# Optimization experiments

Measured on AMD Instinct MI355X. Metric: run time of the kernel, lower is better.

The kernel has to match this reference:

```python
import jax, jax.numpy as jnp
import numpy as np

FILTERS = 64
NBITS = 4
NUE = 4
NSPU = 2
NST = NUE * NSPU           # 8 streams total
OUT_CH = NST * NBITS       # 32 output channels
NBS, NANT = 1, 16
CIN = NBS * NANT * 2 + NBS * NANT * NUE * NSPU * 2 + NUE * NSPU + 1  # 297


def hard_sigmoid(x):
    # Keras ConvLSTM2D default recurrent_activation
    return jnp.clip(0.2 * x + 0.5, 0.0, 1.0)


def conv2d(x, w):
    # x: [N,H,W,C], w: [kh,kw,Cin,Cout], SAME padding
    return jax.lax.conv_general_dilated(x, w, (1, 1), 'SAME',
                                        dimension_numbers=('NHWC', 'HWIO', 'NHWC'))


def convlstm2d(x, Wx, Wh, b):
    """Keras ConvLSTM2D (return_sequences=True), gate order i,f,c,o.
    x: [B,T,H,W,Cin] -> [B,T,H,W,F].
    Input-to-hidden convs are precomputed for all timesteps at once;
    only the cheap hidden-to-hidden conv is inside the scan."""
    B, T, H, W, Cin = x.shape
    F = Wh.shape[2]
    xz = conv2d(x.reshape(B * T, H, W, Cin), Wx).reshape(B, T, H, W, 4 * F) + b
    xz = jnp.moveaxis(xz, 1, 0)  # [T,B,H,W,4F]
    h0 = jnp.zeros((B, H, W, F), x.dtype)

    def step(carry, z_in):
        h, c = carry
        z = z_in + conv2d(h, Wh)
        zi, zf, zg, zo = jnp.split(z, 4, axis=-1)
        i = hard_sigmoid(zi)
        f = hard_sigmoid(zf)
        g = jnp.tanh(zg)
        o = hard_sigmoid(zo)
        c = f * c + i * g
        h = o * jnp.tanh(c)
        return (h, c), h

    _, hs = jax.lax.scan(step, (h0, h0), xz)
    return jnp.moveaxis(hs, 0, 1)  # [B,T,H,W,F]


def _lstm_params(key, cin, f, scale=0.05):
    k1, k2, k3 = jax.random.split(key, 3)
    Wx = jax.random.normal(k1, (3, 3, cin, 4 * f), jnp.float32) * scale
    Wh = jax.random.normal(k2, (3, 3, f, 4 * f), jnp.float32) * scale
    b = jax.random.normal(k3, (4 * f,), jnp.float32) * scale
    return Wx, Wh, b


def setup_inputs() -> dict:
    key = jax.random.key(0)
    ks = jax.random.split(key, 10)
    B, T, W = 2, 14, 1536
    inp = {
        'y_ri': jax.random.normal(ks[0], (B, NBS, NANT, T, W, 2), jnp.float32),
        'h_ri': jax.random.normal(ks[1], (B, NBS, NANT, NUE, NSPU, T, W, 2), jnp.float32),
        'err_var': jax.random.uniform(ks[2], (1, 1, 1, NUE, NSPU, T, W), jnp.float32),
        'no': jax.random.uniform(ks[3], (1,), jnp.float32),
    }
    inp['Wx_in'], inp['Wh_in'], inp['b_in'] = _lstm_params(ks[4], CIN, FILTERS)
    inp['Wx_r0'], inp['Wh_r0'], inp['b_r0'] = _lstm_params(ks[5], FILTERS, FILTERS)
    inp['Wx_r1'], inp['Wh_r1'], inp['b_r1'] = _lstm_params(ks[6], FILTERS, FILTERS)
    inp['Wx_out'], inp['Wh_out'], inp['b_out'] = _lstm_params(ks[7], FILTERS, OUT_CH)
    return inp


def _forward(y_ri, h_ri, err_var, no,
             Wx_in, Wh_in, b_in,
             Wx_r0, Wh_r0, b_r0,
             Wx_r1, Wh_r1, b_r1,
             Wx_out, Wh_out, b_out):
    B, nbs, nant, T, W, _ = y_ri.shape
    # y: [B,nbs,nant,T,W,2] -> [B,T,W,nbs*nant*2]
    y_feats = jnp.transpose(y_ri, (0, 3, 4, 1, 2, 5)).reshape(B, T, W, -1)
    # h: [B,nbs,nant,ue,spu,T,W,2] -> [B,T,W,nbs*nant*ue*spu*2]
    h_feats = jnp.transpose(h_ri, (0, 5, 6, 1, 2, 3, 4, 7)).reshape(B, T, W, -1)
    # err_var: [1,1,1,ue,spu,T,W] -> [B,T,W,ue*spu]
    ev = jnp.transpose(err_var[0, 0, 0], (2, 3, 0, 1)).reshape(1, T, W, NUE * NSPU)
    err_feats = jnp.broadcast_to(ev, (B, T, W, NUE * NSPU))
    no_feat = jnp.broadcast_to(no.reshape(1, 1, 1, 1), (B, T, W, 1))
    z = jnp.concatenate([y_feats, h_feats, err_feats, no_feat], axis=-1)
    z = z[:, :, :, None, :]  # [B,T,W,1,C]

    z = convlstm2d(z, Wx_in, Wh_in, b_in)
    # residual blocks (in_ch == filters, so identity skip)
    z = convlstm2d(z, Wx_r0, Wh_r0, b_r0) + z
    z = convlstm2d(z, Wx_r1, Wh_r1, b_r1) + z
    z = convlstm2d(z, Wx_out, Wh_out, b_out)

    z = z[:, :, :, 0, :]  # [B,T,W,OUT_CH]
    N = T * W
    z = z.reshape(B, N, NUE, NSPU, NBITS)
    z = jnp.transpose(z, (0, 2, 3, 1, 4))
    return z.reshape(B, NUE, NSPU, N * NBITS)


def reference(y_ri, h_ri, err_var, no,
              Wx_in, Wh_in, b_in,
              Wx_r0, Wh_r0, b_r0,
              Wx_r1, Wh_r1, b_r1,
              Wx_out, Wh_out, b_out):
    return _forward(y_ri, h_ri, err_var, no,
                    Wx_in, Wh_in, b_in,
                    Wx_r0, Wh_r0, b_r0,
                    Wx_r1, Wh_r1, b_r1,
                    Wx_out, Wh_out, b_out)
```

## Files before the change

### kernel.cpp

```cpp
#include <hip/hip_runtime.h>
#include <hip/hip_bf16.h>


#define BB   2
#define TT   14
#define LL   1536
#define CINR 297
#define CP_IN 320
#define NSTRIP 96
#define NBLK  (BB * NSTRIP)
#define WIN  48

typedef __attribute__((ext_vector_type(8))) short short8;
typedef __attribute__((ext_vector_type(4))) float floatx4;

static constexpr size_t U_WBIN_HI  = 0;
static constexpr size_t U_WBIN_LO  = 245760;
static constexpr size_t U_WBR0_HI  = 491520;
static constexpr size_t U_WBR0_LO  = 540672;
static constexpr size_t U_WBR1_HI  = 589824;
static constexpr size_t U_WBR1_LO  = 638976;
static constexpr size_t U_WBOUT_HI = 688128;
static constexpr size_t U_WBOUT_LO = 712704;
static constexpr size_t U_WHTIN    = 737280;
static constexpr size_t U_WHTR0    = 786432;
static constexpr size_t U_WHTR1    = 835584;
static constexpr size_t U_WHTOUT   = 884736;
static constexpr size_t OFF_BIN   = 448512;
static constexpr size_t OFF_BR0   = 448768;
static constexpr size_t OFF_BR1   = 449024;
static constexpr size_t OFF_BOUT  = 449280;
static constexpr size_t OFF_Z0HI  = 458752;
static constexpr size_t SZ_Z0PL   = 6881280;
static constexpr size_t OFF_Z0LO  = OFF_Z0HI + SZ_Z0PL;
static constexpr size_t OFF_XZ    = OFF_Z0LO + SZ_Z0PL;
static constexpr size_t SZ_XZ     = (size_t)BB*TT*LL*256;
static constexpr size_t OFF_SEQ   = OFF_Z0HI;
static constexpr size_t OFF_SEQHI = OFF_SEQ + (size_t)BB*TT*LL*64;
static constexpr size_t OFF_SEQLO = OFF_SEQHI + (size_t)BB*TT*LL*32;

__device__ __forceinline__ float hsig(float x) {
    return fminf(fmaxf(0.2f * x + 0.5f, 0.0f), 1.0f);
}
__device__ __forceinline__ float ftanh(float x) {
    float e = __expf(2.0f * x);
    return 1.0f - 2.0f / (e + 1.0f);
}
__device__ __forceinline__ unsigned short f2bf(float x) {
    unsigned int u = __builtin_bit_cast(unsigned int, x);
    u += 0x7fffu + ((u >> 16) & 1u);
    return (unsigned short)(u >> 16);
}
__device__ __forceinline__ float bf2f(unsigned short h) {
    unsigned int u = ((unsigned int)h) << 16;
    return __builtin_bit_cast(float, u);
}

__global__ __launch_bounds__(256)
void prep_weights_kernel(const float* wx_in, const float* wh_in, const float* b_in,
                         const float* wx_r0, const float* wh_r0, const float* b_r0,
                         const float* wx_r1, const float* wh_r1, const float* b_r1,
                         const float* wx_out, const float* wh_out, const float* b_out,
                         float* __restrict__ ws)
{
    int idx = blockIdx.x * 256 + threadIdx.x;
    unsigned short* u = (unsigned short*)ws;
    if (idx < 245760) {
        int n = idx / 960, k = idx % 960;
        int kh = k / CP_IN, ci = k % CP_IN;
        float v = 0.0f;
        if (ci < CINR) {
            int f = n >> 2, g = n & 3;
            v = wx_in[((size_t)(kh * 3 + 1) * CINR + ci) * 256 + g * 64 + f];
        }
        unsigned short hi = f2bf(v);
        u[U_WBIN_HI + idx] = hi;
        u[U_WBIN_LO + idx] = f2bf(v - bf2f(hi));
        return;
    }
    idx -= 245760;
    if (idx < 49152) {
        int n = idx / 192, k = idx % 192;
        int kh = k >> 6, ci = k & 63;
        int f = n >> 2, g = n & 3;
        float v = wx_r0[((size_t)(kh * 3 + 1) * 64 + ci) * 256 + g * 64 + f];
        unsigned short hi = f2bf(v);
        u[U_WBR0_HI + idx] = hi;
        u[U_WBR0_LO + idx] = f2bf(v - bf2f(hi));
        return;
    }
    idx -= 49152;
    if (idx < 49152) {
        int n = idx / 192, k = idx % 192;
        int kh = k >> 6, ci = k & 63;
        int f = n >> 2, g = n & 3;
        float v = wx_r1[((size_t)(kh * 3 + 1) * 64 + ci) * 256 + g * 64 + f];
        unsigned short hi = f2bf(v);
        u[U_WBR1_HI + idx] = hi;
        u[U_WBR1_LO + idx] = f2bf(v - bf2f(hi));
        return;
    }
    idx -= 49152;
    if (idx < 24576) {
        int n = idx / 192, k = idx % 192;
        int kh = k >> 6, ci = k & 63;
        int f = n >> 2, g = n & 3;
        float v = wx_out[((size_t)(kh * 3 + 1) * 64 + ci) * 128 + g * 32 + f];
        unsigned short hi = f2bf(v);
        u[U_WBOUT_HI + idx] = hi;
        u[U_WBOUT_LO + idx] = f2bf(v - bf2f(hi));
        return;
    }
    idx -= 24576;
    if (idx < 49152) {
        int n = idx / 192, k = idx % 192, kh = k >> 6, ci = k & 63;
        u[U_WHTIN + idx] = f2bf(wh_in[((size_t)(kh * 3 + 1) * 64 + ci) * 256 + n]);
        return;
    }
    idx -= 49152;
    if (idx < 49152) {
        int n = idx / 192, k = idx % 192, kh = k >> 6, ci = k & 63;
        u[U_WHTR0 + idx] = f2bf(wh_r0[((size_t)(kh * 3 + 1) * 64 + ci) * 256 + n]);
        return;
    }
    idx -= 49152;
    if (idx < 49152) {
        int n = idx / 192, k = idx % 192, kh = k >> 6, ci = k & 63;
        u[U_WHTR1 + idx] = f2bf(wh_r1[((size_t)(kh * 3 + 1) * 64 + ci) * 256 + n]);
        return;
    }
    idx -= 49152;
    if (idx < 12288) {
        int n = idx / 96, k = idx % 96, kh = k / 32, ci = k % 32;
        u[U_WHTOUT + idx] = f2bf(wh_out[((size_t)(kh * 3 + 1) * 32 + ci) * 128 + n]);
        return;
    }
    idx -= 12288;
    if (idx < 256) { int f = idx >> 2, g = idx & 3; ws[OFF_BIN + idx] = b_in[g * 64 + f]; return; }
    idx -= 256;
    if (idx < 256) { int f = idx >> 2, g = idx & 3; ws[OFF_BR0 + idx] = b_r0[g * 64 + f]; return; }
    idx -= 256;
    if (idx < 256) { int f = idx >> 2, g = idx & 3; ws[OFF_BR1 + idx] = b_r1[g * 64 + f]; return; }
    idx -= 256;
    if (idx < 128) { int f = idx >> 2, g = idx & 3; ws[OFF_BOUT + idx] = b_out[g * 32 + f]; return; }
}

__global__ __launch_bounds__(256)
void build_features_kernel(const float* __restrict__ y,
                           const float* __restrict__ h,
                           const float* __restrict__ ev,
                           const float* __restrict__ no,
                           unsigned short* __restrict__ z0hi,
                           unsigned short* __restrict__ z0lo)
{
    long long idx = (long long)blockIdx.x * 256 + threadIdx.x;
    const long long total = (long long)BB * TT * LL * CP_IN;
    if (idx >= total) return;
    int c = (int)(idx % CP_IN);
    long long rest = idx / CP_IN;
    int l = (int)(rest % LL); rest /= LL;
    int t = (int)(rest % TT);
    int b = (int)(rest / TT);
    float v = 0.0f;
    if (c < 32) {
        int na = c >> 1, ri = c & 1;
        v = y[((((long long)b * 16 + na) * TT + t) * LL + l) * 2 + ri];
    } else if (c < 288) {
        int q = c - 32;
        int ri = q & 1, nspu = (q >> 1) & 1, nue = (q >> 2) & 3, na = q >> 4;
        v = h[((((((long long)b * 16 + na) * 4 + nue) * 2 + nspu) * TT + t) * LL + l) * 2 + ri];
    } else if (c < 296) {
        int q = c - 288; int nspu = q & 1, nue = q >> 1;
        v = ev[(((long long)(nue * 2 + nspu) * TT + t) * LL) + l];
    } else if (c == 296) {
        v = no[0];
    }
    unsigned short hi = f2bf(v);
    z0hi[idx] = hi;
    z0lo[idx] = f2bf(v - bf2f(hi));
}

__global__ __launch_bounds__(256)
void xz_gemm_mfma_kernel(const unsigned short* __restrict__ Ahi,
                         const unsigned short* __restrict__ Alo,
                         int Cpitch,
                         const unsigned short* __restrict__ Bhi,
                         const unsigned short* __restrict__ Blo,
                         const float* __restrict__ bias,
                         float* __restrict__ out, int Ncol)
{
    __shared__ unsigned short AsHi[66 * 40], AsLo[66 * 40];
    const int tid  = threadIdx.x;
    const int lane = tid & 63;
    const int wv   = tid >> 6;
    const int m    = lane & 15;
    const int quad = lane >> 4;
    const int bt   = blockIdx.y;
    const int l0   = blockIdx.x * 64;
    const int n0   = blockIdx.z * 128;
    const int K    = 3 * Cpitch;
    const int NC   = Cpitch >> 5;

    const int aC8   = (tid & 3) * 8;
    const int aRow  = (tid >> 5) * 8 + ((tid >> 2) & 3) * 2 + ((tid >> 4) & 1);
    const int aRowT = 64 + ((tid >> 2) & 1);

    short8 aH0 = (short8)0, aL0 = (short8)0, aH1 = (short8)0, aL1 = (short8)0;

    {
        const int row = l0 + aRow - 1;
        if (row >= 0 && row < LL) {
            size_t off = ((size_t)bt * LL + row) * Cpitch + aC8;
            aH0 = *reinterpret_cast<const short8*>(&Ahi[off]);
            aL0 = *reinterpret_cast<const short8*>(&Alo[off]);
        }
        if (tid < 8) {
            const int rowt = l0 + aRowT - 1;
            if (rowt >= 0 && rowt < LL) {
                size_t off = ((size_t)bt * LL + rowt) * Cpitch + aC8;
                aH1 = *reinterpret_cast<const short8*>(&Ahi[off]);
                aL1 = *reinterpret_cast<const short8*>(&Alo[off]);
            }
        }
    }

    const size_t bBase = (size_t)(n0 + wv * 16 + m) * K + quad * 8;

    floatx4 acc[4][2];
#pragma unroll
    for (int i = 0; i < 4; i++)
#pragma unroll
        for (int j = 0; j < 2; j++) acc[i][j] = (floatx4){0.f, 0.f, 0.f, 0.f};

    for (int cc = 0; cc < NC; ++cc) {
        short8 bh[3][2], bl[3][2];
#pragma unroll
        for (int kh = 0; kh < 3; ++kh)
#pragma unroll
            for (int nt = 0; nt < 2; ++nt) {
                const size_t off = bBase + (size_t)nt * 64 * K
                                 + (size_t)kh * Cpitch + cc * 32;
                bh[kh][nt] = *reinterpret_cast<const short8*>(&Bhi[off]);
                bl[kh][nt] = *reinterpret_cast<const short8*>(&Blo[off]);
            }

        __syncthreads();
        *reinterpret_cast<short8*>(&AsHi[aRow * 40 + aC8]) = aH0;
        *reinterpret_cast<short8*>(&AsLo[aRow * 40 + aC8]) = aL0;
        if (tid < 8) {
            *reinterpret_cast<short8*>(&AsHi[aRowT * 40 + aC8]) = aH1;
            *reinterpret_cast<short8*>(&AsLo[aRowT * 40 + aC8]) = aL1;
        }
        if (cc + 1 < NC) {
            const int c32 = (cc + 1) * 32;
            const int row = l0 + aRow - 1;
            aH0 = (short8)0; aL0 = (short8)0;
            if (row >= 0 && row < LL) {
                size_t off = ((size_t)bt * LL + row) * Cpitch + c32 + aC8;
                aH0 = *reinterpret_cast<const short8*>(&Ahi[off]);
                aL0 = *reinterpret_cast<const short8*>(&Alo[off]);
            }
            if (tid < 8) {
                aH1 = (short8)0; aL1 = (short8)0;
                const int rowt = l0 + aRowT - 1;
                if (rowt >= 0 && rowt < LL) {
                    size_t off = ((size_t)bt * LL + rowt) * Cpitch + c32 + aC8;
                    aH1 = *reinterpret_cast<const short8*>(&Ahi[off]);
                    aL1 = *reinterpret_cast<const short8*>(&Alo[off]);
                }
            }
        }
        __syncthreads();
#pragma unroll
        for (int kh = 0; kh < 3; ++kh) {
#pragma unroll
            for (int mt = 0; mt < 4; ++mt) {
                const int aofs = (mt * 16 + m + kh) * 40 + quad * 8;
                const short8 ah = *reinterpret_cast<const short8*>(&AsHi[aofs]);
                const short8 al = *reinterpret_cast<const short8*>(&AsLo[aofs]);
                acc[mt][0] = __builtin_amdgcn_mfma_f32_16x16x32_bf16(al, bh[kh][0], acc[mt][0], 0, 0, 0);
                acc[mt][0] = __builtin_amdgcn_mfma_f32_16x16x32_bf16(ah, bl[kh][0], acc[mt][0], 0, 0, 0);
                acc[mt][0] = __builtin_amdgcn_mfma_f32_16x16x32_bf16(ah, bh[kh][0], acc[mt][0], 0, 0, 0);
                acc[mt][1] = __builtin_amdgcn_mfma_f32_16x16x32_bf16(al, bh[kh][1], acc[mt][1], 0, 0, 0);
                acc[mt][1] = __builtin_amdgcn_mfma_f32_16x16x32_bf16(ah, bl[kh][1], acc[mt][1], 0, 0, 0);
                acc[mt][1] = __builtin_amdgcn_mfma_f32_16x16x32_bf16(ah, bh[kh][1], acc[mt][1], 0, 0, 0);
            }
        }
    }
#pragma unroll
    for (int nt = 0; nt < 2; ++nt) {
        const int col = n0 + nt * 64 + wv * 16 + m;
        const float bv = bias[col];
#pragma unroll
        for (int mt = 0; mt < 4; ++mt) {
#pragma unroll
            for (int reg = 0; reg < 4; ++reg) {
                int l = l0 + mt * 16 + quad * 4 + reg;
                out[((size_t)bt * LL + l) * Ncol + col] = acc[mt][nt][reg] + bv;
            }
        }
    }
}

template <int F_, bool RESID, bool OUTW>
__global__ __launch_bounds__(64 * (F_ / 16))
void lstm_scan_kernel(const float* __restrict__ xz,
                      const unsigned short* __restrict__ WhT,
                      float* seq,
                      unsigned short* __restrict__ seqhb,
                      unsigned short* __restrict__ seqlb,
                      float* __restrict__ dout)
{
    constexpr int NW = F_ / 16;
    constexpr int NT = 64 * NW;
    constexpr int K  = 3 * F_;
    constexpr int KS = K / 32;
    constexpr int KH = KS / 3;
    constexpr int HP = F_ + 8;
    __shared__ unsigned short Hs[2][(WIN + 2) * HP];

    const int tid  = threadIdx.x;
    const int lane = tid & 63;
    const int wv   = tid >> 6;
    const int m    = lane & 15;
    const int quad = lane >> 4;
    const int blk  = blockIdx.x;
    const int b    = blk / NSTRIP;
    const int o0   = (blk % NSTRIP) * 16;
    const int f    = wv * 16 + m;

    short8 bfr[4][KS];
#pragma unroll
    for (int g = 0; g < 4; g++)
#pragma unroll
        for (int ks = 0; ks < KS; ks++) {
            const int n  = g * F_ + f;
            const int k0 = ks * 32 + quad * 8;
            bfr[g][ks] = *reinterpret_cast<const short8*>(&WhT[(size_t)n * K + k0]);
        }

    for (int idx = tid; idx < (WIN + 2) * HP; idx += NT) {
        Hs[0][idx] = 0; Hs[1][idx] = 0;
    }
    __syncthreads();

    float c[3][4];
#pragma unroll
    for (int i = 0; i < 3; i++)
#pragma unroll
        for (int j = 0; j < 4; j++) c[i][j] = 0.0f;

    int cur = 0;
    for (int t = 0; t < TT; ++t) {
        const size_t btL = ((size_t)b * TT + t) * LL;

        float4 xzv[3][4];
        float  rsv[4];
#pragma unroll
        for (int mt = 0; mt < 3; ++mt)
#pragma unroll
            for (int reg = 0; reg < 4; ++reg) {
                const int w = mt * 16 + quad * 4 + reg;
                const int l = o0 - 16 + w;
                float4 v = make_float4(0.f, 0.f, 0.f, 0.f);
                if (l >= 0 && l < LL && w >= t && w < WIN - t)
                    v = *reinterpret_cast<const float4*>(
                        &xz[(btL + l) * (size_t)(4 * F_) + f * 4]);
                xzv[mt][reg] = v;
            }
        if (RESID) {
#pragma unroll
            for (int reg = 0; reg < 4; ++reg) {
                const int l = o0 + quad * 4 + reg;
                rsv[reg] = seq[(btL + l) * F_ + f];
            }
        }

        const int nxt = cur ^ 1;
#pragma unroll
        for (int mt = 0; mt < 3; ++mt) {
            floatx4 zi = {0.f, 0.f, 0.f, 0.f};
            floatx4 zf = {0.f, 0.f, 0.f, 0.f};
            floatx4 zg = {0.f, 0.f, 0.f, 0.f};
            floatx4 zo = {0.f, 0.f, 0.f, 0.f};
            if (t > 0) {
#pragma unroll
                for (int kh = 0; kh < 3; kh++) {
#pragma unroll
                    for (int hf = 0; hf < KH; hf++) {
                        const short8 af = *reinterpret_cast<const short8*>(
                            &Hs[cur][(mt * 16 + m + kh) * HP + hf * 32 + quad * 8]);
                        const int ks = kh * KH + hf;
                        zi = __builtin_amdgcn_mfma_f32_16x16x32_bf16(af, bfr[0][ks], zi, 0, 0, 0);
                        zf = __builtin_amdgcn_mfma_f32_16x16x32_bf16(af, bfr[1][ks], zf, 0, 0, 0);
                        zg = __builtin_amdgcn_mfma_f32_16x16x32_bf16(af, bfr[2][ks], zg, 0, 0, 0);
                        zo = __builtin_amdgcn_mfma_f32_16x16x32_bf16(af, bfr[3][ks], zo, 0, 0, 0);
                    }
                }
            }
#pragma unroll
            for (int reg = 0; reg < 4; ++reg) {
                const int w = mt * 16 + quad * 4 + reg;
                const int l = o0 - 16 + w;
                const bool valid = (l >= 0 && l < LL);
                const float4 z4 = xzv[mt][reg];
                const float ig = hsig(z4.x + zi[reg]);
                const float fg = hsig(z4.y + zf[reg]);
                const float gg = ftanh(z4.z + zg[reg]);
                const float og = hsig(z4.w + zo[reg]);
                float cn = fg * c[mt][reg] + ig * gg;
                float hn = og * ftanh(cn);
                if (!valid) { cn = 0.0f; hn = 0.0f; }
                c[mt][reg] = cn;
                Hs[nxt][(1 + w) * HP + f] = f2bf(hn);
                if (w >= 16 && w < 32) {
                    if (OUTW) {
                        const int ue = f >> 3, spu = (f >> 2) & 1, bit = f & 3;
                        const size_t n = (size_t)t * LL + l;
                        dout[(((size_t)b * 4 + ue) * 2 + spu) * ((size_t)TT * LL * 4)
                             + n * 4 + bit] = hn;
                    } else {
                        float v = hn;
                        if (RESID) v += rsv[reg];
                        seq[(btL + l) * F_ + f] = v;
                        const unsigned short hi = f2bf(v);
                        seqhb[(btL + l) * F_ + f] = hi;
                        seqlb[(btL + l) * F_ + f] = f2bf(v - bf2f(hi));
                    }
                }
            }
        }
        __syncthreads();
        cur = nxt;
    }
}

extern "C" void kernel_launch(void* const* d_in, const int* in_sizes, int n_in,
                              void* d_out, int out_size, void* d_ws, size_t ws_size,
                              hipStream_t stream)
{
    (void)in_sizes; (void)n_in; (void)out_size; (void)ws_size;
    const float* y_ri   = (const float*)d_in[0];
    const float* h_ri   = (const float*)d_in[1];
    const float* evar   = (const float*)d_in[2];
    const float* no     = (const float*)d_in[3];
    const float* wx_in  = (const float*)d_in[4];
    const float* wh_in  = (const float*)d_in[5];
    const float* b_in   = (const float*)d_in[6];
    const float* wx_r0  = (const float*)d_in[7];
    const float* wh_r0  = (const float*)d_in[8];
    const float* b_r0   = (const float*)d_in[9];
    const float* wx_r1  = (const float*)d_in[10];
    const float* wh_r1  = (const float*)d_in[11];
    const float* b_r1   = (const float*)d_in[12];
    const float* wx_out = (const float*)d_in[13];
    const float* wh_out = (const float*)d_in[14];
    const float* b_out  = (const float*)d_in[15];

    float* ws = (float*)d_ws;
    unsigned short* wu = (unsigned short*)d_ws;
    float* dout = (float*)d_out;

    prep_weights_kernel<<<2068, 256, 0, stream>>>(
        wx_in, wh_in, b_in, wx_r0, wh_r0, b_r0,
        wx_r1, wh_r1, b_r1, wx_out, wh_out, b_out, ws);
    {
        long long total = (long long)BB * TT * LL * CP_IN;
        int blocks = (int)((total + 255) / 256);
        build_features_kernel<<<blocks, 256, 0, stream>>>(
            y_ri, h_ri, evar, no,
            (unsigned short*)(ws + OFF_Z0HI), (unsigned short*)(ws + OFF_Z0LO));
    }

    float* xz    = ws + OFF_XZ;
    float* seq   = ws + OFF_SEQ;
    unsigned short* seqhb = (unsigned short*)(ws + OFF_SEQHI);
    unsigned short* seqlb = (unsigned short*)(ws + OFF_SEQLO);

    const dim3 gIn(LL / 64, BB * TT, 2);
    const dim3 gO (LL / 64, BB * TT, 1);

    xz_gemm_mfma_kernel<<<gIn, 256, 0, stream>>>(
        (unsigned short*)(ws + OFF_Z0HI), (unsigned short*)(ws + OFF_Z0LO), CP_IN,
        wu + U_WBIN_HI, wu + U_WBIN_LO, ws + OFF_BIN, xz, 256);
    lstm_scan_kernel<64, false, false><<<NBLK, 256, 0, stream>>>(
        xz, wu + U_WHTIN, seq, seqhb, seqlb, nullptr);

    xz_gemm_mfma_kernel<<<gIn, 256, 0, stream>>>(
        seqhb, seqlb, 64, wu + U_WBR0_HI, wu + U_WBR0_LO, ws + OFF_BR0, xz, 256);
    lstm_scan_kernel<64, true, false><<<NBLK, 256, 0, stream>>>(
        xz, wu + U_WHTR0, seq, seqhb, seqlb, nullptr);

    xz_gemm_mfma_kernel<<<gIn, 256, 0, stream>>>(
        seqhb, seqlb, 64, wu + U_WBR1_HI, wu + U_WBR1_LO, ws + OFF_BR1, xz, 256);
    lstm_scan_kernel<64, true, false><<<NBLK, 256, 0, stream>>>(
        xz, wu + U_WHTR1, seq, seqhb, seqlb, nullptr);

    xz_gemm_mfma_kernel<<<gO, 256, 0, stream>>>(
        seqhb, seqlb, 64, wu + U_WBOUT_HI, wu + U_WBOUT_LO, ws + OFF_BOUT, xz, 128);
    lstm_scan_kernel<32, false, true><<<NBLK, 128, 0, stream>>>(
        xz, wu + U_WHTOUT, nullptr, nullptr, nullptr, dout);
}
```

Measured before the change: 502.7 us.

## Double-buffer xz GEMM LDS and B registers, template on channel pitch

Restructures the input-to-hidden GEMM kernel so the A tile in LDS and the B weight fragments in registers are double-buffered. The next chunk's global loads are issued before the current chunk's MFMAs, which removes one barrier per chunk and hides load latency. The channel pitch becomes a template parameter, giving compile-time loop bounds, and launch bounds request two blocks per CU. The cost is twice the LDS and more registers, which could limit occupancy.

```diff
diff --git a/kernel.cpp b/kernel.cpp
--- a/kernel.cpp
+++ b/kernel.cpp
@@ -180,16 +180,72 @@
     z0lo[idx] = f2bf(v - bf2f(hi));
 }
 
-__global__ __launch_bounds__(256)
+
+#define GEMM_CHUNK(CC, P)                                                      \
+    {                                                                          \
+        const int ccn = (CC) + 1;                                              \
+        if (ccn < NC) {                                                        \
+            const int c32 = ccn * 32;                                          \
+            aH0n = (short8)0; aL0n = (short8)0;                                \
+            if (av) {                                                          \
+                aH0n = *reinterpret_cast<const short8*>(&Ahi[aBase + c32]);    \
+                aL0n = *reinterpret_cast<const short8*>(&Alo[aBase + c32]);    \
+            }                                                                  \
+            if (tid < 8) {                                                     \
+                aH1n = (short8)0; aL1n = (short8)0;                            \
+                if (atv) {                                                     \
+                    aH1n = *reinterpret_cast<const short8*>(&Ahi[aBaseT + c32]); \
+                    aL1n = *reinterpret_cast<const short8*>(&Alo[aBaseT + c32]); \
+                }                                                              \
+            }                                                                  \
+            _Pragma("unroll")                                                  \
+            for (int kh = 0; kh < 3; ++kh)                                     \
+                _Pragma("unroll")                                              \
+                for (int nt = 0; nt < 2; ++nt) {                               \
+                    const size_t off = bBase + (size_t)nt * 64 * K             \
+                                     + (size_t)kh * CP + c32;                  \
+                    bh[(P) ^ 1][kh][nt] = *reinterpret_cast<const short8*>(&Bhi[off]); \
+                    bl[(P) ^ 1][kh][nt] = *reinterpret_cast<const short8*>(&Blo[off]); \
+                }                                                              \
+        }                                                                      \
+        _Pragma("unroll")                                                      \
+        for (int kh = 0; kh < 3; ++kh) {                                       \
+            _Pragma("unroll")                                                  \
+            for (int mt = 0; mt < 4; ++mt) {                                   \
+                const int aofs = (mt * 16 + m + kh) * 40 + quad * 8;           \
+                const short8 ah = *reinterpret_cast<const short8*>(&AsHi[(P)][aofs]); \
+                const short8 al = *reinterpret_cast<const short8*>(&AsLo[(P)][aofs]); \
+                acc[mt][0] = __builtin_amdgcn_mfma_f32_16x16x32_bf16(al, bh[(P)][kh][0], acc[mt][0], 0, 0, 0); \
+                acc[mt][0] = __builtin_amdgcn_mfma_f32_16x16x32_bf16(ah, bl[(P)][kh][0], acc[mt][0], 0, 0, 0); \
+                acc[mt][0] = __builtin_amdgcn_mfma_f32_16x16x32_bf16(ah, bh[(P)][kh][0], acc[mt][0], 0, 0, 0); \
+                acc[mt][1] = __builtin_amdgcn_mfma_f32_16x16x32_bf16(al, bh[(P)][kh][1], acc[mt][1], 0, 0, 0); \
+                acc[mt][1] = __builtin_amdgcn_mfma_f32_16x16x32_bf16(ah, bl[(P)][kh][1], acc[mt][1], 0, 0, 0); \
+                acc[mt][1] = __builtin_amdgcn_mfma_f32_16x16x32_bf16(ah, bh[(P)][kh][1], acc[mt][1], 0, 0, 0); \
+            }                                                                  \
+        }                                                                      \
+        if (ccn < NC) {                                                        \
+            *reinterpret_cast<short8*>(&AsHi[(P) ^ 1][aSlot]) = aH0n;          \
+            *reinterpret_cast<short8*>(&AsLo[(P) ^ 1][aSlot]) = aL0n;          \
+            if (tid < 8) {                                                     \
+                *reinterpret_cast<short8*>(&AsHi[(P) ^ 1][aSlotT]) = aH1n;     \
+                *reinterpret_cast<short8*>(&AsLo[(P) ^ 1][aSlotT]) = aL1n;     \
+            }                                                                  \
+            __syncthreads();                                                   \
+        }                                                                      \
+    }
+
+template <int CP>
+__global__ __launch_bounds__(256, 2)
 void xz_gemm_mfma_kernel(const unsigned short* __restrict__ Ahi,
                          const unsigned short* __restrict__ Alo,
-                         int Cpitch,
                          const unsigned short* __restrict__ Bhi,
                          const unsigned short* __restrict__ Blo,
                          const float* __restrict__ bias,
                          float* __restrict__ out, int Ncol)
 {
-    __shared__ unsigned short AsHi[66 * 40], AsLo[66 * 40];
+    constexpr int NC = CP / 32;
+    constexpr int K  = 3 * CP;
+    __shared__ unsigned short AsHi[2][66 * 40], AsLo[2][66 * 40];
     const int tid  = threadIdx.x;
     const int lane = tid & 63;
     const int wv   = tid >> 6;
@@ -198,33 +254,47 @@
     const int bt   = blockIdx.y;
     const int l0   = blockIdx.x * 64;
     const int n0   = blockIdx.z * 128;
-    const int K    = 3 * Cpitch;
-    const int NC   = Cpitch >> 5;
 
     const int aC8   = (tid & 3) * 8;
     const int aRow  = (tid >> 5) * 8 + ((tid >> 2) & 3) * 2 + ((tid >> 4) & 1);
     const int aRowT = 64 + ((tid >> 2) & 1);
-
-    short8 aH0 = (short8)0, aL0 = (short8)0, aH1 = (short8)0, aL1 = (short8)0;
-
-    {
-        const int row = l0 + aRow - 1;
-        if (row >= 0 && row < LL) {
-            size_t off = ((size_t)bt * LL + row) * Cpitch + aC8;
-            aH0 = *reinterpret_cast<const short8*>(&Ahi[off]);
-            aL0 = *reinterpret_cast<const short8*>(&Alo[off]);
+    const int aSlot  = aRow * 40 + aC8;
+    const int aSlotT = aRowT * 40 + aC8;
+    const int arow_g  = l0 + aRow - 1;
+    const int arowt_g = l0 + aRowT - 1;
+    const bool av  = (arow_g >= 0 && arow_g < LL);
+    const bool atv = (arowt_g < LL);
+    const long long aBase  = ((long long)bt * LL + arow_g) * CP + aC8;
+    const long long aBaseT = ((long long)bt * LL + arowt_g) * CP + aC8;
+
+    const size_t bBase = (size_t)(n0 + wv * 16 + m) * K + quad * 8;
+
+    short8 aH0n = (short8)0, aL0n = (short8)0, aH1n = (short8)0, aL1n = (short8)0;
+    short8 bh[2][3][2], bl[2][3][2];
+
+    if (av) {
+        aH0n = *reinterpret_cast<const short8*>(&Ahi[aBase]);
+        aL0n = *reinterpret_cast<const short8*>(&Alo[aBase]);
+    }
+    if (tid < 8 && atv) {
+        aH1n = *reinterpret_cast<const short8*>(&Ahi[aBaseT]);
+        aL1n = *reinterpret_cast<const short8*>(&Alo[aBaseT]);
+    }
+#pragma unroll
+    for (int kh = 0; kh < 3; ++kh)
+#pragma unroll
+        for (int nt = 0; nt < 2; ++nt) {
+            const size_t off = bBase + (size_t)nt * 64 * K + (size_t)kh * CP;
+            bh[0][kh][nt] = *reinterpret_cast<const short8*>(&Bhi[off]);
+            bl[0][kh][nt] = *reinterpret_cast<const short8*>(&Blo[off]);
         }
-        if (tid < 8) {
-            const int rowt = l0 + aRowT - 1;
-            if (rowt >= 0 && rowt < LL) {
-                size_t off = ((size_t)bt * LL + rowt) * Cpitch + aC8;
-                aH1 = *reinterpret_cast<const short8*>(&Ahi[off]);
-                aL1 = *reinterpret_cast<const short8*>(&Alo[off]);
-            }
-        }
-    }
-
-    const size_t bBase = (size_t)(n0 + wv * 16 + m) * K + quad * 8;
+    *reinterpret_cast<short8*>(&AsHi[0][aSlot]) = aH0n;
+    *reinterpret_cast<short8*>(&AsLo[0][aSlot]) = aL0n;
+    if (tid < 8) {
+        *reinterpret_cast<short8*>(&AsHi[0][aSlotT]) = aH1n;
+        *reinterpret_cast<short8*>(&AsLo[0][aSlotT]) = aL1n;
+    }
+    __syncthreads();
 
     floatx4 acc[4][2];
 #pragma unroll
@@ -232,61 +302,12 @@
 #pragma unroll
         for (int j = 0; j < 2; j++) acc[i][j] = (floatx4){0.f, 0.f, 0.f, 0.f};
 
-    for (int cc = 0; cc < NC; ++cc) {
-        short8 bh[3][2], bl[3][2];
-#pragma unroll
-        for (int kh = 0; kh < 3; ++kh)
-#pragma unroll
-            for (int nt = 0; nt < 2; ++nt) {
-                const size_t off = bBase + (size_t)nt * 64 * K
-                                 + (size_t)kh * Cpitch + cc * 32;
-                bh[kh][nt] = *reinterpret_cast<const short8*>(&Bhi[off]);
-                bl[kh][nt] = *reinterpret_cast<const short8*>(&Blo[off]);
-            }
-
-        __syncthreads();
-        *reinterpret_cast<short8*>(&AsHi[aRow * 40 + aC8]) = aH0;
-        *reinterpret_cast<short8*>(&AsLo[aRow * 40 + aC8]) = aL0;
-        if (tid < 8) {
-            *reinterpret_cast<short8*>(&AsHi[aRowT * 40 + aC8]) = aH1;
-            *reinterpret_cast<short8*>(&AsLo[aRowT * 40 + aC8]) = aL1;
-        }
-        if (cc + 1 < NC) {
-            const int c32 = (cc + 1) * 32;
-            const int row = l0 + aRow - 1;
-            aH0 = (short8)0; aL0 = (short8)0;
-            if (row >= 0 && row < LL) {
-                size_t off = ((size_t)bt * LL + row) * Cpitch + c32 + aC8;
-                aH0 = *reinterpret_cast<const short8*>(&Ahi[off]);
-                aL0 = *reinterpret_cast<const short8*>(&Alo[off]);
-            }
-            if (tid < 8) {
-                aH1 = (short8)0; aL1 = (short8)0;
-                const int rowt = l0 + aRowT - 1;
-                if (rowt >= 0 && rowt < LL) {
-                    size_t off = ((size_t)bt * LL + rowt) * Cpitch + c32 + aC8;
-                    aH1 = *reinterpret_cast<const short8*>(&Ahi[off]);
-                    aL1 = *reinterpret_cast<const short8*>(&Alo[off]);
-                }
-            }
-        }
-        __syncthreads();
-#pragma unroll
-        for (int kh = 0; kh < 3; ++kh) {
-#pragma unroll
-            for (int mt = 0; mt < 4; ++mt) {
-                const int aofs = (mt * 16 + m + kh) * 40 + quad * 8;
-                const short8 ah = *reinterpret_cast<const short8*>(&AsHi[aofs]);
-                const short8 al = *reinterpret_cast<const short8*>(&AsLo[aofs]);
-                acc[mt][0] = __builtin_amdgcn_mfma_f32_16x16x32_bf16(al, bh[kh][0], acc[mt][0], 0, 0, 0);
-                acc[mt][0] = __builtin_amdgcn_mfma_f32_16x16x32_bf16(ah, bl[kh][0], acc[mt][0], 0, 0, 0);
-                acc[mt][0] = __builtin_amdgcn_mfma_f32_16x16x32_bf16(ah, bh[kh][0], acc[mt][0], 0, 0, 0);
-                acc[mt][1] = __builtin_amdgcn_mfma_f32_16x16x32_bf16(al, bh[kh][1], acc[mt][1], 0, 0, 0);
-                acc[mt][1] = __builtin_amdgcn_mfma_f32_16x16x32_bf16(ah, bl[kh][1], acc[mt][1], 0, 0, 0);
-                acc[mt][1] = __builtin_amdgcn_mfma_f32_16x16x32_bf16(ah, bh[kh][1], acc[mt][1], 0, 0, 0);
-            }
-        }
-    }
+#pragma unroll 1
+    for (int cc0 = 0; cc0 < NC; cc0 += 2) {
+        GEMM_CHUNK(cc0, 0)
+        GEMM_CHUNK(cc0 + 1, 1)
+    }
+
 #pragma unroll
     for (int nt = 0; nt < 2; ++nt) {
         const int col = n0 + nt * 64 + wv * 16 + m;
@@ -301,6 +322,7 @@
         }
     }
 }
+#undef GEMM_CHUNK
 
 template <int F_, bool RESID, bool OUTW>
 __global__ __launch_bounds__(64 * (F_ / 16))
@@ -480,24 +502,24 @@
     const dim3 gIn(LL / 64, BB * TT, 2);
     const dim3 gO (LL / 64, BB * TT, 1);
 
-    xz_gemm_mfma_kernel<<<gIn, 256, 0, stream>>>(
-        (unsigned short*)(ws + OFF_Z0HI), (unsigned short*)(ws + OFF_Z0LO), CP_IN,
+    xz_gemm_mfma_kernel<CP_IN><<<gIn, 256, 0, stream>>>(
+        (unsigned short*)(ws + OFF_Z0HI), (unsigned short*)(ws + OFF_Z0LO),
         wu + U_WBIN_HI, wu + U_WBIN_LO, ws + OFF_BIN, xz, 256);
     lstm_scan_kernel<64, false, false><<<NBLK, 256, 0, stream>>>(
         xz, wu + U_WHTIN, seq, seqhb, seqlb, nullptr);
 
-    xz_gemm_mfma_kernel<<<gIn, 256, 0, stream>>>(
-        seqhb, seqlb, 64, wu + U_WBR0_HI, wu + U_WBR0_LO, ws + OFF_BR0, xz, 256);
+    xz_gemm_mfma_kernel<64><<<gIn, 256, 0, stream>>>(
+        seqhb, seqlb, wu + U_WBR0_HI, wu + U_WBR0_LO, ws + OFF_BR0, xz, 256);
     lstm_scan_kernel<64, true, false><<<NBLK, 256, 0, stream>>>(
         xz, wu + U_WHTR0, seq, seqhb, seqlb, nullptr);
 
-    xz_gemm_mfma_kernel<<<gIn, 256, 0, stream>>>(
-        seqhb, seqlb, 64, wu + U_WBR1_HI, wu + U_WBR1_LO, ws + OFF_BR1, xz, 256);
+    xz_gemm_mfma_kernel<64><<<gIn, 256, 0, stream>>>(
+        seqhb, seqlb, wu + U_WBR1_HI, wu + U_WBR1_LO, ws + OFF_BR1, xz, 256);
     lstm_scan_kernel<64, true, false><<<NBLK, 256, 0, stream>>>(
         xz, wu + U_WHTR1, seq, seqhb, seqlb, nullptr);
 
-    xz_gemm_mfma_kernel<<<gO, 256, 0, stream>>>(
-        seqhb, seqlb, 64, wu + U_WBOUT_HI, wu + U_WBOUT_LO, ws + OFF_BOUT, xz, 128);
+    xz_gemm_mfma_kernel<64><<<gO, 256, 0, stream>>>(
+        seqhb, seqlb, wu + U_WBOUT_HI, wu + U_WBOUT_LO, ws + OFF_BOUT, xz, 128);
     lstm_scan_kernel<32, false, true><<<NBLK, 128, 0, stream>>>(
         xz, wu + U_WHTOUT, nullptr, nullptr, nullptr, dout);
 }
```

Result: no change. 509.8 us (+1.4%).

## Pad activation rows with zero halos and load GEMM A operands directly from global

Applied to the files above, without the earlier changes.

Activation buffers (input features and the hidden-sequence bf16 splits) gain one zero row on each side of every (b,t) slice, written by two small zeroing kernels. With the halo in place, the xz GEMM drops its LDS staging, its two barriers per chunk and its bounds checks, and each wave loads its A fragments straight from global memory into registers. The kernel is also templated on channel pitch and given a min-blocks-per-CU launch bound. The intent is to remove LDS round-trips and synchronisation, at the cost of redundant global/L2 reads of overlapping rows across waves, more registers, and two extra small launches.

```diff
diff --git a/kernel.cpp b/kernel.cpp
--- a/kernel.cpp
+++ b/kernel.cpp
@@ -5,6 +5,7 @@
 #define BB   2
 #define TT   14
 #define LL   1536
+#define LL2  1538
 #define CINR 297
 #define CP_IN 320
 #define NSTRIP 96
@@ -31,13 +32,13 @@
 static constexpr size_t OFF_BR1   = 449024;
 static constexpr size_t OFF_BOUT  = 449280;
 static constexpr size_t OFF_Z0HI  = 458752;
-static constexpr size_t SZ_Z0PL   = 6881280;
+static constexpr size_t SZ_Z0PL   = 6890240;
 static constexpr size_t OFF_Z0LO  = OFF_Z0HI + SZ_Z0PL;
 static constexpr size_t OFF_XZ    = OFF_Z0LO + SZ_Z0PL;
 static constexpr size_t SZ_XZ     = (size_t)BB*TT*LL*256;
 static constexpr size_t OFF_SEQ   = OFF_Z0HI;
-static constexpr size_t OFF_SEQHI = OFF_SEQ + (size_t)BB*TT*LL*64;
-static constexpr size_t OFF_SEQLO = OFF_SEQHI + (size_t)BB*TT*LL*32;
+static constexpr size_t OFF_SEQHI = OFF_SEQ + (size_t)BB*TT*LL2*64;
+static constexpr size_t OFF_SEQLO = OFF_SEQHI + (size_t)BB*TT*LL2*32;
 
 __device__ __forceinline__ float hsig(float x) {
     return fminf(fmaxf(0.2f * x + 0.5f, 0.0f), 1.0f);
@@ -54,6 +55,34 @@
 __device__ __forceinline__ float bf2f(unsigned short h) {
     unsigned int u = ((unsigned int)h) << 16;
     return __builtin_bit_cast(float, u);
+}
+
+__global__ __launch_bounds__(256)
+void zero_pads_kernel(unsigned short* __restrict__ z0hi,
+                      unsigned short* __restrict__ z0lo)
+{
+    int idx = blockIdx.x * 256 + threadIdx.x;
+    const int NZ = BB * TT * 2 * CP_IN;
+    if (idx < NZ) {
+        int c = idx % CP_IN, r2 = idx / CP_IN;
+        int p = r2 >> 1, e = r2 & 1;
+        long long off = ((long long)p * LL2 + (e ? (LL2 - 1) : 0)) * CP_IN + c;
+        z0hi[off] = 0; z0lo[off] = 0;
+    }
+}
+
+__global__ __launch_bounds__(256)
+void zero_seq_pads_kernel(unsigned short* __restrict__ seqhb,
+                          unsigned short* __restrict__ seqlb)
+{
+    int idx = blockIdx.x * 256 + threadIdx.x;
+    const int NS = BB * TT * 2 * 64;
+    if (idx < NS) {
+        int c = idx % 64, r2 = idx / 64;
+        int p = r2 >> 1, e = r2 & 1;
+        long long off = ((long long)p * LL2 + (e ? (LL2 - 1) : 0)) * 64 + c;
+        seqhb[off] = 0; seqlb[off] = 0;
+    }
 }
 
 __global__ __launch_bounds__(256)
@@ -175,21 +204,23 @@
     } else if (c == 296) {
         v = no[0];
     }
+    const long long widx = (((long long)(b * TT + t)) * LL2 + (l + 1)) * CP_IN + c;
     unsigned short hi = f2bf(v);
-    z0hi[idx] = hi;
-    z0lo[idx] = f2bf(v - bf2f(hi));
-}
-
-__global__ __launch_bounds__(256)
+    z0hi[widx] = hi;
+    z0lo[widx] = f2bf(v - bf2f(hi));
+}
+
+template <int CP>
+__global__ __launch_bounds__(256, 2)
 void xz_gemm_mfma_kernel(const unsigned short* __restrict__ Ahi,
                          const unsigned short* __restrict__ Alo,
-                         int Cpitch,
                          const unsigned short* __restrict__ Bhi,
                          const unsigned short* __restrict__ Blo,
                          const float* __restrict__ bias,
                          float* __restrict__ out, int Ncol)
 {
-    __shared__ unsigned short AsHi[66 * 40], AsLo[66 * 40];
+    constexpr int NC = CP / 32;
+    constexpr int K  = 3 * CP;
     const int tid  = threadIdx.x;
     const int lane = tid & 63;
     const int wv   = tid >> 6;
@@ -198,33 +229,9 @@
     const int bt   = blockIdx.y;
     const int l0   = blockIdx.x * 64;
     const int n0   = blockIdx.z * 128;
-    const int K    = 3 * Cpitch;
-    const int NC   = Cpitch >> 5;
-
-    const int aC8   = (tid & 3) * 8;
-    const int aRow  = (tid >> 5) * 8 + ((tid >> 2) & 3) * 2 + ((tid >> 4) & 1);
-    const int aRowT = 64 + ((tid >> 2) & 1);
-
-    short8 aH0 = (short8)0, aL0 = (short8)0, aH1 = (short8)0, aL1 = (short8)0;
-
-    {
-        const int row = l0 + aRow - 1;
-        if (row >= 0 && row < LL) {
-            size_t off = ((size_t)bt * LL + row) * Cpitch + aC8;
-            aH0 = *reinterpret_cast<const short8*>(&Ahi[off]);
-            aL0 = *reinterpret_cast<const short8*>(&Alo[off]);
-        }
-        if (tid < 8) {
-            const int rowt = l0 + aRowT - 1;
-            if (rowt >= 0 && rowt < LL) {
-                size_t off = ((size_t)bt * LL + rowt) * Cpitch + aC8;
-                aH1 = *reinterpret_cast<const short8*>(&Ahi[off]);
-                aL1 = *reinterpret_cast<const short8*>(&Alo[off]);
-            }
-        }
-    }
-
-    const size_t bBase = (size_t)(n0 + wv * 16 + m) * K + quad * 8;
+
+    const long long aBase = ((long long)bt * LL2 + l0 + m) * CP + quad * 8;
+    const size_t    bBase = (size_t)(n0 + wv * 16 + m) * K + quad * 8;
 
     floatx4 acc[4][2];
 #pragma unroll
@@ -232,61 +239,41 @@
 #pragma unroll
         for (int j = 0; j < 2; j++) acc[i][j] = (floatx4){0.f, 0.f, 0.f, 0.f};
 
+#pragma unroll 1
     for (int cc = 0; cc < NC; ++cc) {
+        const int c32 = cc * 32;
+        short8 ah[4][3], al[4][3];
+#pragma unroll
+        for (int mt = 0; mt < 4; ++mt)
+#pragma unroll
+            for (int kh = 0; kh < 3; ++kh) {
+                const long long off = aBase + (long long)(mt * 16 + kh) * CP + c32;
+                ah[mt][kh] = *reinterpret_cast<const short8*>(&Ahi[off]);
+                al[mt][kh] = *reinterpret_cast<const short8*>(&Alo[off]);
+            }
         short8 bh[3][2], bl[3][2];
 #pragma unroll
         for (int kh = 0; kh < 3; ++kh)
 #pragma unroll
             for (int nt = 0; nt < 2; ++nt) {
-                const size_t off = bBase + (size_t)nt * 64 * K
-                                 + (size_t)kh * Cpitch + cc * 32;
+                const size_t off = bBase + (size_t)nt * 64 * K + (size_t)kh * CP + c32;
                 bh[kh][nt] = *reinterpret_cast<const short8*>(&Bhi[off]);
                 bl[kh][nt] = *reinterpret_cast<const short8*>(&Blo[off]);
             }
-
-        __syncthreads();
-        *reinterpret_cast<short8*>(&AsHi[aRow * 40 + aC8]) = aH0;
-        *reinterpret_cast<short8*>(&AsLo[aRow * 40 + aC8]) = aL0;
-        if (tid < 8) {
-            *reinterpret_cast<short8*>(&AsHi[aRowT * 40 + aC8]) = aH1;
-            *reinterpret_cast<short8*>(&AsLo[aRowT * 40 + aC8]) = aL1;
-        }
-        if (cc + 1 < NC) {
-            const int c32 = (cc + 1) * 32;
-            const int row = l0 + aRow - 1;
-            aH0 = (short8)0; aL0 = (short8)0;
-            if (row >= 0 && row < LL) {
-                size_t off = ((size_t)bt * LL + row) * Cpitch + c32 + aC8;
-                aH0 = *reinterpret_cast<const short8*>(&Ahi[off]);
-                aL0 = *reinterpret_cast<const short8*>(&Alo[off]);
-            }
-            if (tid < 8) {
-                aH1 = (short8)0; aL1 = (short8)0;
-                const int rowt = l0 + aRowT - 1;
-                if (rowt >= 0 && rowt < LL) {
-                    size_t off = ((size_t)bt * LL + rowt) * Cpitch + c32 + aC8;
-                    aH1 = *reinterpret_cast<const short8*>(&Ahi[off]);
-                    aL1 = *reinterpret_cast<const short8*>(&Alo[off]);
-                }
-            }
-        }
-        __syncthreads();
 #pragma unroll
         for (int kh = 0; kh < 3; ++kh) {
 #pragma unroll
             for (int mt = 0; mt < 4; ++mt) {
-                const int aofs = (mt * 16 + m + kh) * 40 + quad * 8;
-                const short8 ah = *reinterpret_cast<const short8*>(&AsHi[aofs]);
-                const short8 al = *reinterpret_cast<const short8*>(&AsLo[aofs]);
-                acc[mt][0] = __builtin_amdgcn_mfma_f32_16x16x32_bf16(al, bh[kh][0], acc[mt][0], 0, 0, 0);
-                acc[mt][0] = __builtin_amdgcn_mfma_f32_16x16x32_bf16(ah, bl[kh][0], acc[mt][0], 0, 0, 0);
-                acc[mt][0] = __builtin_amdgcn_mfma_f32_16x16x32_bf16(ah, bh[kh][0], acc[mt][0], 0, 0, 0);
-                acc[mt][1] = __builtin_amdgcn_mfma_f32_16x16x32_bf16(al, bh[kh][1], acc[mt][1], 0, 0, 0);
-                acc[mt][1] = __builtin_amdgcn_mfma_f32_16x16x32_bf16(ah, bl[kh][1], acc[mt][1], 0, 0, 0);
-                acc[mt][1] = __builtin_amdgcn_mfma_f32_16x16x32_bf16(ah, bh[kh][1], acc[mt][1], 0, 0, 0);
-            }
-        }
-    }
+                acc[mt][0] = __builtin_amdgcn_mfma_f32_16x16x32_bf16(al[mt][kh], bh[kh][0], acc[mt][0], 0, 0, 0);
+                acc[mt][0] = __builtin_amdgcn_mfma_f32_16x16x32_bf16(ah[mt][kh], bl[kh][0], acc[mt][0], 0, 0, 0);
+                acc[mt][0] = __builtin_amdgcn_mfma_f32_16x16x32_bf16(ah[mt][kh], bh[kh][0], acc[mt][0], 0, 0, 0);
+                acc[mt][1] = __builtin_amdgcn_mfma_f32_16x16x32_bf16(al[mt][kh], bh[kh][1], acc[mt][1], 0, 0, 0);
+                acc[mt][1] = __builtin_amdgcn_mfma_f32_16x16x32_bf16(ah[mt][kh], bl[kh][1], acc[mt][1], 0, 0, 0);
+                acc[mt][1] = __builtin_amdgcn_mfma_f32_16x16x32_bf16(ah[mt][kh], bh[kh][1], acc[mt][1], 0, 0, 0);
+            }
+        }
+    }
+
 #pragma unroll
     for (int nt = 0; nt < 2; ++nt) {
         const int col = n0 + nt * 64 + wv * 16 + m;
@@ -352,7 +339,8 @@
 
     int cur = 0;
     for (int t = 0; t < TT; ++t) {
-        const size_t btL = ((size_t)b * TT + t) * LL;
+        const size_t btL  = ((size_t)b * TT + t) * LL;
+        const size_t btLP = ((size_t)b * TT + t) * LL2;
 
         float4 xzv[3][4];
         float  rsv[4];
@@ -372,7 +360,7 @@
 #pragma unroll
             for (int reg = 0; reg < 4; ++reg) {
                 const int l = o0 + quad * 4 + reg;
-                rsv[reg] = seq[(btL + l) * F_ + f];
+                rsv[reg] = seq[(btLP + 1 + l) * F_ + f];
             }
         }
 
@@ -422,10 +410,10 @@
                     } else {
                         float v = hn;
                         if (RESID) v += rsv[reg];
-                        seq[(btL + l) * F_ + f] = v;
+                        seq[(btLP + 1 + l) * F_ + f] = v;
                         const unsigned short hi = f2bf(v);
-                        seqhb[(btL + l) * F_ + f] = hi;
-                        seqlb[(btL + l) * F_ + f] = f2bf(v - bf2f(hi));
+                        seqhb[(btLP + 1 + l) * F_ + f] = hi;
+                        seqlb[(btLP + 1 + l) * F_ + f] = f2bf(v - bf2f(hi));
                     }
                 }
             }
@@ -461,6 +449,14 @@
     unsigned short* wu = (unsigned short*)d_ws;
     float* dout = (float*)d_out;
 
+    unsigned short* z0hi = (unsigned short*)(ws + OFF_Z0HI);
+    unsigned short* z0lo = (unsigned short*)(ws + OFF_Z0LO);
+    float* xz    = ws + OFF_XZ;
+    float* seq   = ws + OFF_SEQ;
+    unsigned short* seqhb = (unsigned short*)(ws + OFF_SEQHI);
+    unsigned short* seqlb = (unsigned short*)(ws + OFF_SEQLO);
+
+    zero_pads_kernel<<<70, 256, 0, stream>>>(z0hi, z0lo);
     prep_weights_kernel<<<2068, 256, 0, stream>>>(
         wx_in, wh_in, b_in, wx_r0, wh_r0, b_r0,
         wx_r1, wh_r1, b_r1, wx_out, wh_out, b_out, ws);
@@ -468,36 +464,30 @@
         long long total = (long long)BB * TT * LL * CP_IN;
         int blocks = (int)((total + 255) / 256);
         build_features_kernel<<<blocks, 256, 0, stream>>>(
-            y_ri, h_ri, evar, no,
-            (unsigned short*)(ws + OFF_Z0HI), (unsigned short*)(ws + OFF_Z0LO));
-    }
-
-    float* xz    = ws + OFF_XZ;
-    float* seq   = ws + OFF_SEQ;
-    unsigned short* seqhb = (unsigned short*)(ws + OFF_SEQHI);
-    unsigned short* seqlb = (unsigned short*)(ws + OFF_SEQLO);
+            y_ri, h_ri, evar, no, z0hi, z0lo);
+    }
 
     const dim3 gIn(LL / 64, BB * TT, 2);
     const dim3 gO (LL / 64, BB * TT, 1);
 
-    xz_gemm_mfma_kernel<<<gIn, 256, 0, stream>>>(
-        (unsigned short*)(ws + OFF_Z0HI), (unsigned short*)(ws + OFF_Z0LO), CP_IN,
-        wu + U_WBIN_HI, wu + U_WBIN_LO, ws + OFF_BIN, xz, 256);
+    xz_gemm_mfma_kernel<CP_IN><<<gIn, 256, 0, stream>>>(
+        z0hi, z0lo, wu + U_WBIN_HI, wu + U_WBIN_LO, ws + OFF_BIN, xz, 256);
+    zero_seq_pads_kernel<<<14, 256, 0, stream>>>(seqhb, seqlb);
     lstm_scan_kernel<64, false, false><<<NBLK, 256, 0, stream>>>(
         xz, wu + U_WHTIN, seq, seqhb, seqlb, nullptr);
 
-    xz_gemm_mfma_kernel<<<gIn, 256, 0, stream>>>(
-        seqhb, seqlb, 64, wu + U_WBR0_HI, wu + U_WBR0_LO, ws + OFF_BR0, xz, 256);
+    xz_gemm_mfma_kernel<64><<<gIn, 256, 0, stream>>>(
+        seqhb, seqlb, wu + U_WBR0_HI, wu + U_WBR0_LO, ws + OFF_BR0, xz, 256);
     lstm_scan_kernel<64, true, false><<<NBLK, 256, 0, stream>>>(
         xz, wu + U_WHTR0, seq, seqhb, seqlb, nullptr);
 
-    xz_gemm_mfma_kernel<<<gIn, 256, 0, stream>>>(
-        seqhb, seqlb, 64, wu + U_WBR1_HI, wu + U_WBR1_LO, ws + OFF_BR1, xz, 256);
+    xz_gemm_mfma_kernel<64><<<gIn, 256, 0, stream>>>(
+        seqhb, seqlb, wu + U_WBR1_HI, wu + U_WBR1_LO, ws + OFF_BR1, xz, 256);
     lstm_scan_kernel<64, true, false><<<NBLK, 256, 0, stream>>>(
         xz, wu + U_WHTR1, seq, seqhb, seqlb, nullptr);
 
-    xz_gemm_mfma_kernel<<<gO, 256, 0, stream>>>(
-        seqhb, seqlb, 64, wu + U_WBOUT_HI, wu + U_WBOUT_LO, ws + OFF_BOUT, xz, 128);
+    xz_gemm_mfma_kernel<64><<<gO, 256, 0, stream>>>(
+        seqhb, seqlb, wu + U_WBOUT_HI, wu + U_WBOUT_LO, ws + OFF_BOUT, xz, 128);
     lstm_scan_kernel<32, false, true><<<NBLK, 128, 0, stream>>>(
         xz, wu + U_WHTOUT, nullptr, nullptr, nullptr, dout);
 }
```

Result: slower. 719.6 us (+43.1%).
